# Performance work log

Measured on AMD Instinct MI355X. Metric: run time of the kernel, lower is better.

The kernel has to match this reference:

```python
import jax, jax.numpy as jnp
import numpy as np

N, E, D, H_ATT = 10000, 640000, 128, 64


def setup_inputs() -> dict:
    key = jax.random.key(0)
    ks = jax.random.split(key, 8)
    s = 1.0 / np.sqrt(D)
    return {
        "x": jax.random.normal(ks[0], (N, D), jnp.float32),
        "row": jax.random.randint(ks[1], (E,), 0, N, dtype=jnp.int32),
        "col": jax.random.randint(ks[2], (E,), 0, N, dtype=jnp.int32),
        "W1": jax.random.normal(ks[3], (D, D), jnp.float32) * s,
        "b1": jnp.zeros((D,), jnp.float32),
        "W2": jax.random.normal(ks[4], (D, D), jnp.float32) * s,
        "b2": jnp.zeros((D,), jnp.float32),
        "A1": jax.random.normal(ks[5], (D, H_ATT), jnp.float32) * s,
        "ab1": jnp.zeros((H_ATT,), jnp.float32),
        "A2": jax.random.normal(ks[6], (H_ATT, 1), jnp.float32) * (1.0 / np.sqrt(H_ATT)),
    }


def _cos_sim(a, b):
    # torch.cosine_similarity with eps=1e-8
    num = jnp.sum(a * b, axis=-1)
    den = jnp.maximum(jnp.linalg.norm(a, axis=-1) * jnp.linalg.norm(b, axis=-1), 1e-8)
    return num / den


def _euclid(a, b):
    # nn.PairwiseDistance(p=2)
    return jnp.sqrt(jnp.sum((a - b) ** 2, axis=-1) + 1e-12)


def _gcn(x, ew, row, col, W, b):
    # PyG GCNConv: add self loops (weight 1), symmetric normalization, SpMM.
    n = x.shape[0]
    loop = jnp.arange(n, dtype=row.dtype)
    r = jnp.concatenate([row, loop])  # target
    c = jnp.concatenate([col, loop])  # source
    w = jnp.concatenate([ew, jnp.ones((n,), x.dtype)])
    deg = jax.ops.segment_sum(w, r, num_segments=n)
    dis = jnp.where(deg > 0, jax.lax.rsqrt(jnp.maximum(deg, 1e-12)), 0.0)
    norm = dis[r] * w * dis[c]  # [E+N]
    h = x @ W  # [N, out]
    out = jax.ops.segment_sum(norm[:, None] * h[c], r, num_segments=n)
    return out + b


def reference(x, row, col, W1, b1, W2, b2, A1, ab1, A2):
    # --- cosine branch ---
    w = _cos_sim(x[row], x[col])
    x1 = jax.nn.relu(_gcn(x, w, row, col, W1, b1))
    w = _cos_sim(x1[row], x1[col])
    x1 = _gcn(x1, w, row, col, W2, b2)
    # --- euclidean branch ---
    w = _euclid(x[row], x[col])
    x2 = jax.nn.relu(_gcn(x, w, row, col, W1, b1))
    w = _euclid(x2[row], x2[col])
    x2 = _gcn(x2, w, row, col, W2, b2)
    # --- semantic attention fusion ---
    emb = jnp.stack([x1, x2], axis=1)  # [N, 2, D]
    score = jnp.tanh(emb @ A1 + ab1) @ A2  # [N, 2, 1]
    beta = jax.nn.softmax(score, axis=1)
    return jnp.sum(beta * emb, axis=1)  # [N, D]
```

## Files before the change

kernel.cpp:

```cpp
#include <hip/hip_runtime.h>
#include <cstdint>
#include <cstddef>

#define DF 128
#define HATT 64
#define SL 64
#define RPB 1280

static inline int divup(int a, int b) { return (a + b - 1) / b; }

typedef int vint4 __attribute__((ext_vector_type(4)));

__global__ __launch_bounds__(256) void hist2_kernel(const int* __restrict__ row,
                                                    int* __restrict__ cnt2,
                                                    int E, int n, int ranges, int rpb, int es) {
    int rb = blockIdx.x % ranges;
    int s  = blockIdx.x / ranges;
    int lo = rb * rpb, hi = min(lo + rpb, n);
    int rows = hi - lo;
    __shared__ int lc[RPB];
    for (int j = threadIdx.x; j < rows; j += 256) lc[j] = 0;
    __syncthreads();
    int i0 = s * es, i1 = min(i0 + es, E);
    const vint4* rv = (const vint4*)row;
    for (int j = i0 / 4 + threadIdx.x; j < i1 / 4; j += 256) {
        vint4 r4 = __builtin_nontemporal_load(rv + j);
        if (r4.x >= lo && r4.x < hi) atomicAdd(&lc[r4.x - lo], 1);
        if (r4.y >= lo && r4.y < hi) atomicAdd(&lc[r4.y - lo], 1);
        if (r4.z >= lo && r4.z < hi) atomicAdd(&lc[r4.z - lo], 1);
        if (r4.w >= lo && r4.w < hi) atomicAdd(&lc[r4.w - lo], 1);
    }
    __syncthreads();
    for (int j = threadIdx.x; j < rows; j += 256) cnt2[(size_t)s * n + lo + j] = lc[j];
}

__global__ __launch_bounds__(256) void scanRT_kernel(int* __restrict__ cnt2,
                                                     int* __restrict__ tot, int n) {
    __shared__ int tile[SL][65];
    int r0 = blockIdx.x * 64;
    int w = threadIdx.x >> 6;
    int lane = threadIdx.x & 63;
    int rows = min(64, n - r0);
    for (int s = w; s < SL; s += 4) {
        int v = (lane < rows) ? cnt2[(size_t)s * n + r0 + lane] : 0;
        tile[s][lane] = v;
    }
    __syncthreads();
    int t = threadIdx.x;
    if (t < rows) {
        int run = 0;
#pragma unroll
        for (int s = 0; s < SL; ++s) {
            int v = tile[s][t];
            tile[s][t] = run;
            run += v;
        }
        tot[r0 + t] = run;
    }
    __syncthreads();
    for (int s = w; s < SL; s += 4) {
        if (lane < rows) cnt2[(size_t)s * n + r0 + lane] = tile[s][lane];
    }
}

__global__ __launch_bounds__(1024) void scanT_kernel(const int* __restrict__ tot,
                                                     int* __restrict__ row_ptr, int n) {
    __shared__ int sums[1024];
    int t = threadIdx.x;
    int chunk = (n + 1023) >> 10;
    int start = t * chunk, end = min(start + chunk, n);
    int s = 0;
    for (int r = start; r < end; ++r) s += tot[r];
    sums[t] = s;
    __syncthreads();
    for (int off = 1; off < 1024; off <<= 1) {
        int v = (t >= off) ? sums[t - off] : 0;
        __syncthreads();
        sums[t] += v;
        __syncthreads();
    }
    int run = sums[t] - s;
    for (int r = start; r < end; ++r) {
        row_ptr[r] = run;
        run += tot[r];
    }
    if (t == 1023) row_ptr[n] = sums[1023];
}

__global__ __launch_bounds__(256) void scatter2_kernel(const int* __restrict__ row,
                                                       const int* __restrict__ col,
                                                       const int* __restrict__ cnt2,
                                                       const int* __restrict__ row_ptr,
                                                       unsigned short* __restrict__ col_s,
                                                       int E, int n, int ranges, int rpb, int es) {
    int rb = blockIdx.x % ranges;
    int s  = blockIdx.x / ranges;
    int lo = rb * rpb, hi = min(lo + rpb, n);
    int rows = hi - lo;
    __shared__ int cur[RPB];
    for (int j = threadIdx.x; j < rows; j += 256)
        cur[j] = cnt2[(size_t)s * n + lo + j] + row_ptr[lo + j];
    __syncthreads();
    int i0 = s * es, i1 = min(i0 + es, E);
    const vint4* rv = (const vint4*)row;
    const vint4* cv = (const vint4*)col;
    for (int j = i0 / 4 + threadIdx.x; j < i1 / 4; j += 256) {
        vint4 r4 = __builtin_nontemporal_load(rv + j);
        bool b0 = (r4.x >= lo && r4.x < hi);
        bool b1 = (r4.y >= lo && r4.y < hi);
        bool b2 = (r4.z >= lo && r4.z < hi);
        bool b3 = (r4.w >= lo && r4.w < hi);
        if (b0 | b1 | b2 | b3) {
            vint4 c4 = __builtin_nontemporal_load(cv + j);
            if (b0) { int p = atomicAdd(&cur[r4.x - lo], 1); col_s[p] = (unsigned short)c4.x; }
            if (b1) { int p = atomicAdd(&cur[r4.y - lo], 1); col_s[p] = (unsigned short)c4.y; }
            if (b2) { int p = atomicAdd(&cur[r4.z - lo], 1); col_s[p] = (unsigned short)c4.z; }
            if (b3) { int p = atomicAdd(&cur[r4.w - lo], 1); col_s[p] = (unsigned short)c4.w; }
        }
    }
}

__global__ __launch_bounds__(256) void split_x_kernel(const float* __restrict__ x,
                                                      float* __restrict__ xA,
                                                      float* __restrict__ xB,
                                                      float* __restrict__ sqn, int n) {
    int wid = (blockIdx.x * blockDim.x + threadIdx.x) >> 6;
    int lane = threadIdx.x & 63;
    if (wid >= n) return;
    float v0 = x[(size_t)wid * DF + lane];
    float v1 = x[(size_t)wid * DF + 64 + lane];
    xA[(size_t)wid * 64 + lane] = v0;
    xB[(size_t)wid * 64 + lane] = v1;
    float s = v0 * v0 + v1 * v1;
    for (int off = 32; off; off >>= 1) s += __shfl_xor(s, off);
    if (lane == 0) sqn[wid] = s;
}


__global__ __launch_bounds__(256) void edgewA_kernel(const float* __restrict__ tA,
                                                     const unsigned short* __restrict__ col_s,
                                                     const int* __restrict__ row_ptr,
                                                     float* __restrict__ dpart, int n) {
    int wid = (blockIdx.x * blockDim.x + threadIdx.x) >> 6;
    int lane = threadIdx.x & 63;
    if (wid >= n) return;
    int sub = lane & 15, g = lane >> 4;
    int s = row_ptr[wid], e = row_ptr[wid + 1];
    float4 a = ((const float4*)(tA + (size_t)wid * 64))[sub];
    for (int base = s; base < e; base += 64) {
        int m = e - base; if (m > 64) m = 64;
        int cc = 0;
        if (lane < m) cc = (int)col_s[base + lane];
        float dkeep = 0.f;
#define EWA_BODY(CHK)                                                        \
        _Pragma("unroll")                                                    \
        for (int it = 0; it < 16; ++it) {                                    \
            int idx = g * 16 + it;                                           \
            int c = __shfl(cc, idx);                                         \
            if (CHK) {                                                       \
                float4 b = ((const float4*)(tA + (size_t)c * 64))[sub];      \
                float d = a.x * b.x + a.y * b.y + a.z * b.z + a.w * b.w;     \
                d += __shfl_xor(d, 8); d += __shfl_xor(d, 4);                \
                d += __shfl_xor(d, 2); d += __shfl_xor(d, 1);                \
                dkeep = (sub == it) ? d : dkeep;                             \
            }                                                                \
        }
        if (m == 64) { EWA_BODY(true) } else { EWA_BODY(idx < m) }
#undef EWA_BODY
        if (lane < m) dpart[base + lane] = dkeep;
    }
}

__global__ __launch_bounds__(256) void edgewB1_kernel(const float* __restrict__ tB,
                                                      const float* __restrict__ sqn,
                                                      const unsigned short* __restrict__ col_s,
                                                      const int* __restrict__ row_ptr,
                                                      const float* __restrict__ dpart,
                                                      float* __restrict__ wA,
                                                      float* __restrict__ wB,
                                                      float* __restrict__ disA,
                                                      float* __restrict__ disB, int n) {
    int wid = (blockIdx.x * blockDim.x + threadIdx.x) >> 6;
    int lane = threadIdx.x & 63;
    if (wid >= n) return;
    int sub = lane & 15, g = lane >> 4;
    int s = row_ptr[wid], e = row_ptr[wid + 1];
    float4 a = ((const float4*)(tB + (size_t)wid * 64))[sub];
    float na = sqn[wid];
    float accA = 0.f, accB = 0.f;
    for (int base = s; base < e; base += 64) {
        int m = e - base; if (m > 64) m = 64;
        int cc = 0; float dp = 0.f;
        if (lane < m) {
            cc = (int)col_s[base + lane];
            dp = dpart[base + lane];
        }
        float dkeep = 0.f;
#define EWB1_BODY(CHK)                                                       \
        _Pragma("unroll")                                                    \
        for (int it = 0; it < 16; ++it) {                                    \
            int idx = g * 16 + it;                                           \
            int c = __shfl(cc, idx);                                         \
            if (CHK) {                                                       \
                float4 b = ((const float4*)(tB + (size_t)c * 64))[sub];      \
                float d = a.x * b.x + a.y * b.y + a.z * b.z + a.w * b.w;     \
                d += __shfl_xor(d, 8); d += __shfl_xor(d, 4);                \
                d += __shfl_xor(d, 2); d += __shfl_xor(d, 1);                \
                dkeep = (sub == it) ? d : dkeep;                             \
            }                                                                \
        }
        if (m == 64) { EWB1_BODY(true) } else { EWB1_BODY(idx < m) }
#undef EWB1_BODY
        if (lane < m) {
            float d = dkeep + dp;
            float nb = sqn[cc];
            float cw = d / fmaxf(sqrtf(na * nb), 1e-8f);
            float ew = sqrtf(fmaxf(na + nb - 2.f * d, 0.f) + 1e-12f);
            wA[base + lane] = cw;
            wB[base + lane] = ew;
            accA += cw;
            accB += ew;
        }
    }
#pragma unroll
    for (int off = 32; off; off >>= 1) {
        accA += __shfl_xor(accA, off);
        accB += __shfl_xor(accB, off);
    }
    if (lane == 0) {
        float dA = 1.f + accA;
        disA[wid] = (dA > 0.f) ? rsqrtf(fmaxf(dA, 1e-12f)) : 0.f;
        float dB = 1.f + accB;
        disB[wid] = (dB > 0.f) ? rsqrtf(fmaxf(dB, 1e-12f)) : 0.f;
    }
}

__global__ __launch_bounds__(256) void edgewA2_kernel(const float* __restrict__ t0,
                                                      const float* __restrict__ t1,
                                                      const unsigned short* __restrict__ col_s,
                                                      const int* __restrict__ row_ptr,
                                                      float* __restrict__ dp0,
                                                      float* __restrict__ dp1, int n) {
    int br = blockIdx.x & 1;
    int wid = (blockIdx.x >> 1) * 4 + (threadIdx.x >> 6);
    int lane = threadIdx.x & 63;
    if (wid >= n) return;
    const float* tA = br ? t1 : t0;
    float* dpart = br ? dp1 : dp0;
    int sub = lane & 15, g = lane >> 4;
    int s = row_ptr[wid], e = row_ptr[wid + 1];
    float4 a = ((const float4*)(tA + (size_t)wid * 64))[sub];
    for (int base = s; base < e; base += 64) {
        int m = e - base; if (m > 64) m = 64;
        int cc = 0;
        if (lane < m) cc = (int)col_s[base + lane];
        float dkeep = 0.f;
#define EWA2_BODY(CHK)                                                       \
        _Pragma("unroll")                                                    \
        for (int it = 0; it < 16; ++it) {                                    \
            int idx = g * 16 + it;                                           \
            int c = __shfl(cc, idx);                                         \
            if (CHK) {                                                       \
                float4 b = ((const float4*)(tA + (size_t)c * 64))[sub];      \
                float d = a.x * b.x + a.y * b.y + a.z * b.z + a.w * b.w;     \
                d += __shfl_xor(d, 8); d += __shfl_xor(d, 4);                \
                d += __shfl_xor(d, 2); d += __shfl_xor(d, 1);                \
                dkeep = (sub == it) ? d : dkeep;                             \
            }                                                                \
        }
        if (m == 64) { EWA2_BODY(true) } else { EWA2_BODY(idx < m) }
#undef EWA2_BODY
        if (lane < m) dpart[base + lane] = dkeep;
    }
}

__global__ __launch_bounds__(256) void edgewB2_kernel(const float* __restrict__ t0B,
                                                      const float* __restrict__ t1B,
                                                      const float* __restrict__ sq1pA,
                                                      const float* __restrict__ sq1pB,
                                                      const float* __restrict__ sq2pA,
                                                      const float* __restrict__ sq2pB,
                                                      const unsigned short* __restrict__ col_s,
                                                      const int* __restrict__ row_ptr,
                                                      const float* __restrict__ dp0,
                                                      const float* __restrict__ dp1,
                                                      float* __restrict__ wsA,
                                                      float* __restrict__ wsB,
                                                      float* __restrict__ disA,
                                                      float* __restrict__ disB, int n) {
    int br = blockIdx.x & 1;
    int wid = (blockIdx.x >> 1) * 4 + (threadIdx.x >> 6);
    int lane = threadIdx.x & 63;
    if (wid >= n) return;
    const float* tB = br ? t1B : t0B;
    const float* sqA = br ? sq2pA : sq1pA;
    const float* sqB = br ? sq2pB : sq1pB;
    const float* dpart = br ? dp1 : dp0;
    float* wOut = br ? wsB : wsA;
    float* disOut = br ? disB : disA;
    int sub = lane & 15, g = lane >> 4;
    int s = row_ptr[wid], e = row_ptr[wid + 1];
    float4 a = ((const float4*)(tB + (size_t)wid * 64))[sub];
    float na = sqA[wid] + sqB[wid];
    float acc = 0.f;
    for (int base = s; base < e; base += 64) {
        int m = e - base; if (m > 64) m = 64;
        int cc = 0; float dp = 0.f;
        if (lane < m) {
            cc = (int)col_s[base + lane];
            dp = dpart[base + lane];
        }
        float dkeep = 0.f;
#define EWB2_BODY(CHK)                                                       \
        _Pragma("unroll")                                                    \
        for (int it = 0; it < 16; ++it) {                                    \
            int idx = g * 16 + it;                                           \
            int c = __shfl(cc, idx);                                         \
            if (CHK) {                                                       \
                float4 b = ((const float4*)(tB + (size_t)c * 64))[sub];      \
                float d = a.x * b.x + a.y * b.y + a.z * b.z + a.w * b.w;     \
                d += __shfl_xor(d, 8); d += __shfl_xor(d, 4);                \
                d += __shfl_xor(d, 2); d += __shfl_xor(d, 1);                \
                dkeep = (sub == it) ? d : dkeep;                             \
            }                                                                \
        }
        if (m == 64) { EWB2_BODY(true) } else { EWB2_BODY(idx < m) }
#undef EWB2_BODY
        if (lane < m) {
            float d = dkeep + dp;
            float nb = sqA[cc] + sqB[cc];
            float w;
            if (br == 0) w = d / fmaxf(sqrtf(na * nb), 1e-8f);
            else w = sqrtf(fmaxf(na + nb - 2.f * d, 0.f) + 1e-12f);
            wOut[base + lane] = w;
            acc += w;
        }
    }
#pragma unroll
    for (int off = 32; off; off >>= 1) acc += __shfl_xor(acc, off);
    if (lane == 0) {
        float dg = 1.f + acc;
        disOut[wid] = (dg > 0.f) ? rsqrtf(fmaxf(dg, 1e-12f)) : 0.f;
    }
}

__global__ __launch_bounds__(256) void mm_kernel(const float* __restrict__ inA,
                                                 const float* __restrict__ inB,
                                                 int strideIn,
                                                 const float* __restrict__ W,
                                                 float* __restrict__ hA,
                                                 float* __restrict__ hB, int n) {
    int wid = (blockIdx.x * blockDim.x + threadIdx.x) >> 6;
    int lane = threadIdx.x & 63;
    int i0 = wid * 4;
    if (i0 >= n) return;
    float v0[4], v1[4];
#pragma unroll
    for (int r = 0; r < 4; ++r) {
        int i = i0 + r;
        if (i < n) { v0[r] = inA[(size_t)i * strideIn + lane]; v1[r] = inB[(size_t)i * strideIn + lane]; }
        else { v0[r] = 0.f; v1[r] = 0.f; }
    }
    float acc0[4] = {0.f, 0.f, 0.f, 0.f};
    float acc1[4] = {0.f, 0.f, 0.f, 0.f};
#pragma unroll 4
    for (int k = 0; k < 64; ++k) {
        float w0 = W[k * DF + lane];
        float w1 = W[k * DF + 64 + lane];
#pragma unroll
        for (int r = 0; r < 4; ++r) {
            float a = __shfl(v0[r], k);
            acc0[r] = fmaf(a, w0, acc0[r]);
            acc1[r] = fmaf(a, w1, acc1[r]);
        }
    }
#pragma unroll 4
    for (int k = 0; k < 64; ++k) {
        float w0 = W[(k + 64) * DF + lane];
        float w1 = W[(k + 64) * DF + 64 + lane];
#pragma unroll
        for (int r = 0; r < 4; ++r) {
            float a = __shfl(v1[r], k);
            acc0[r] = fmaf(a, w0, acc0[r]);
            acc1[r] = fmaf(a, w1, acc1[r]);
        }
    }
#pragma unroll
    for (int r = 0; r < 4; ++r) {
        int i = i0 + r;
        if (i < n) { hA[(size_t)i * 64 + lane] = acc0[r]; hB[(size_t)i * 64 + lane] = acc1[r]; }
    }
}

__global__ __launch_bounds__(256) void mm2_kernel(const float* __restrict__ x1A_,
                                                  const float* __restrict__ x1B_,
                                                  const float* __restrict__ x2A_,
                                                  const float* __restrict__ x2B_,
                                                  const float* __restrict__ W,
                                                  float* __restrict__ h1A, float* __restrict__ h1B,
                                                  float* __restrict__ h2A, float* __restrict__ h2B,
                                                  int n) {
    int br = blockIdx.x & 1;
    const float* inA = br ? x2A_ : x1A_;
    const float* inB = br ? x2B_ : x1B_;
    float* hA = br ? h2A : h1A;
    float* hB = br ? h2B : h1B;
    int wid = (blockIdx.x >> 1) * 4 + (threadIdx.x >> 6);
    int lane = threadIdx.x & 63;
    int i0 = wid * 4;
    if (i0 >= n) return;
    float v0[4], v1[4];
#pragma unroll
    for (int r = 0; r < 4; ++r) {
        int i = i0 + r;
        if (i < n) { v0[r] = inA[(size_t)i * 64 + lane]; v1[r] = inB[(size_t)i * 64 + lane]; }
        else { v0[r] = 0.f; v1[r] = 0.f; }
    }
    float acc0[4] = {0.f, 0.f, 0.f, 0.f};
    float acc1[4] = {0.f, 0.f, 0.f, 0.f};
#pragma unroll 4
    for (int k = 0; k < 64; ++k) {
        float w0 = W[k * DF + lane];
        float w1 = W[k * DF + 64 + lane];
#pragma unroll
        for (int r = 0; r < 4; ++r) {
            float a = __shfl(v0[r], k);
            acc0[r] = fmaf(a, w0, acc0[r]);
            acc1[r] = fmaf(a, w1, acc1[r]);
        }
    }
#pragma unroll 4
    for (int k = 0; k < 64; ++k) {
        float w0 = W[(k + 64) * DF + lane];
        float w1 = W[(k + 64) * DF + 64 + lane];
#pragma unroll
        for (int r = 0; r < 4; ++r) {
            float a = __shfl(v1[r], k);
            acc0[r] = fmaf(a, w0, acc0[r]);
            acc1[r] = fmaf(a, w1, acc1[r]);
        }
    }
#pragma unroll
    for (int r = 0; r < 4; ++r) {
        int i = i0 + r;
        if (i < n) { hA[(size_t)i * 64 + lane] = acc0[r]; hB[(size_t)i * 64 + lane] = acc1[r]; }
    }
}

__global__ __launch_bounds__(256) void spmm_l1_kernel(const float* __restrict__ hA,
                                                      const float* __restrict__ hB,
                                                      const float* __restrict__ wsA,
                                                      const float* __restrict__ wsB,
                                                      const unsigned short* __restrict__ col_s,
                                                      const float* __restrict__ disA,
                                                      const float* __restrict__ disB,
                                                      const int* __restrict__ row_ptr,
                                                      const float* __restrict__ bias,
                                                      float* __restrict__ x1A, float* __restrict__ x1B,
                                                      float* __restrict__ x2A, float* __restrict__ x2B,
                                                      float* __restrict__ sq1pA, float* __restrict__ sq1pB,
                                                      float* __restrict__ sq2pA, float* __restrict__ sq2pB,
                                                      int n) {
    int half = blockIdx.x & 1;
    int wid = (blockIdx.x >> 1) * 4 + (threadIdx.x >> 6);
    int lane = threadIdx.x & 63;
    if (wid >= n) return;
    const float* hH = half ? hB : hA;
    float* x1H = half ? x1B : x1A;
    float* x2H = half ? x2B : x2A;
    float* sq1 = half ? sq1pB : sq1pA;
    float* sq2 = half ? sq2pB : sq2pA;
    const float* biasH = bias + half * 64;
    int sub = lane & 15, g = lane >> 4;
    int s = row_ptr[wid], e = row_ptr[wid + 1];
    float diA = disA[wid], diB = disB[wid];
    float4 aA = make_float4(0.f, 0.f, 0.f, 0.f);
    float4 aB = make_float4(0.f, 0.f, 0.f, 0.f);
    for (int base = s; base < e; base += 64) {
        int m = e - base; if (m > 64) m = 64;
        int cc = 0; float wa = 0.f, wb = 0.f;
        if (lane < m) {
            cc = (int)col_s[base + lane];
            wa = wsA[base + lane] * disA[cc];
            wb = wsB[base + lane] * disB[cc];
        }
#define SPL1_BODY(CHK)                                                       \
        _Pragma("unroll")                                                    \
        for (int it = 0; it < 16; ++it) {                                    \
            int idx = it * 4 + g;                                            \
            int c = __shfl(cc, idx);                                         \
            float ceA = __shfl(wa, idx);                                     \
            float ceB = __shfl(wb, idx);                                     \
            if (CHK) {                                                       \
                float4 gv = ((const float4*)(hH + (size_t)c * 64))[sub];     \
                aA.x = fmaf(ceA, gv.x, aA.x); aA.y = fmaf(ceA, gv.y, aA.y);  \
                aA.z = fmaf(ceA, gv.z, aA.z); aA.w = fmaf(ceA, gv.w, aA.w);  \
                aB.x = fmaf(ceB, gv.x, aB.x); aB.y = fmaf(ceB, gv.y, aB.y);  \
                aB.z = fmaf(ceB, gv.z, aB.z); aB.w = fmaf(ceB, gv.w, aB.w);  \
            }                                                                \
        }
        if (m == 64) { SPL1_BODY(true) } else { SPL1_BODY(idx < m) }
#undef SPL1_BODY
    }
#pragma unroll
    for (int off = 16; off <= 32; off <<= 1) {
        aA.x += __shfl_xor(aA.x, off); aA.y += __shfl_xor(aA.y, off);
        aA.z += __shfl_xor(aA.z, off); aA.w += __shfl_xor(aA.w, off);
        aB.x += __shfl_xor(aB.x, off); aB.y += __shfl_xor(aB.y, off);
        aB.z += __shfl_xor(aB.z, off); aB.w += __shfl_xor(aB.w, off);
    }
    float4 hv = ((const float4*)(hH + (size_t)wid * 64))[sub];
    float4 bb = ((const float4*)biasH)[sub];
    float4 oA, oB;
    oA.x = fmaxf(diA * (aA.x + diA * hv.x) + bb.x, 0.f);
    oA.y = fmaxf(diA * (aA.y + diA * hv.y) + bb.y, 0.f);
    oA.z = fmaxf(diA * (aA.z + diA * hv.z) + bb.z, 0.f);
    oA.w = fmaxf(diA * (aA.w + diA * hv.w) + bb.w, 0.f);
    oB.x = fmaxf(diB * (aB.x + diB * hv.x) + bb.x, 0.f);
    oB.y = fmaxf(diB * (aB.y + diB * hv.y) + bb.y, 0.f);
    oB.z = fmaxf(diB * (aB.z + diB * hv.z) + bb.z, 0.f);
    oB.w = fmaxf(diB * (aB.w + diB * hv.w) + bb.w, 0.f);
    if (g == 0) {
        ((float4*)(x1H + (size_t)wid * 64))[sub] = oA;
        ((float4*)(x2H + (size_t)wid * 64))[sub] = oB;
    }
    float sA = oA.x * oA.x + oA.y * oA.y + oA.z * oA.z + oA.w * oA.w;
    float sB = oB.x * oB.x + oB.y * oB.y + oB.z * oB.z + oB.w * oB.w;
#pragma unroll
    for (int off = 8; off; off >>= 1) {
        sA += __shfl_xor(sA, off);
        sB += __shfl_xor(sB, off);
    }
    if (lane == 0) { sq1[wid] = sA; sq2[wid] = sB; }
}

__global__ __launch_bounds__(256) void spmm2q_kernel(const float* __restrict__ h1A,
                                                     const float* __restrict__ h1B,
                                                     const float* __restrict__ h2A,
                                                     const float* __restrict__ h2B,
                                                     const float* __restrict__ wsA,
                                                     const float* __restrict__ wsB,
                                                     const unsigned short* __restrict__ col_s,
                                                     const float* __restrict__ disA,
                                                     const float* __restrict__ disB,
                                                     const int* __restrict__ row_ptr,
                                                     const float* __restrict__ bias,
                                                     float* __restrict__ x1A, float* __restrict__ x1B,
                                                     float* __restrict__ x2A, float* __restrict__ x2B,
                                                     int n) {
    int sel = blockIdx.x & 3;
    int br = sel & 1;
    int half = sel >> 1;
    const float* hH = br ? (half ? h2B : h2A) : (half ? h1B : h1A);
    const float* ws = br ? wsB : wsA;
    const float* dis = br ? disB : disA;
    float* outH = br ? (half ? x2B : x2A) : (half ? x1B : x1A);
    const float* biasH = bias + half * 64;
    int wid = (blockIdx.x >> 2) * 4 + (threadIdx.x >> 6);
    int lane = threadIdx.x & 63;
    if (wid >= n) return;
    int sub = lane & 15, g = lane >> 4;
    int s = row_ptr[wid], e = row_ptr[wid + 1];
    float di = dis[wid];
    float4 a = make_float4(0.f, 0.f, 0.f, 0.f);
    for (int base = s; base < e; base += 64) {
        int m = e - base; if (m > 64) m = 64;
        int cc = 0; float wv = 0.f;
        if (lane < m) {
            cc = (int)col_s[base + lane];
            wv = ws[base + lane] * dis[cc];
        }
#define SP2_BODY(CHK)                                                        \
        _Pragma("unroll")                                                    \
        for (int it = 0; it < 16; ++it) {                                    \
            int idx = it * 4 + g;                                            \
            int c = __shfl(cc, idx);                                         \
            float ce = __shfl(wv, idx);                                      \
            if (CHK) {                                                       \
                float4 gv = ((const float4*)(hH + (size_t)c * 64))[sub];     \
                a.x = fmaf(ce, gv.x, a.x); a.y = fmaf(ce, gv.y, a.y);        \
                a.z = fmaf(ce, gv.z, a.z); a.w = fmaf(ce, gv.w, a.w);        \
            }                                                                \
        }
        if (m == 64) { SP2_BODY(true) } else { SP2_BODY(idx < m) }
#undef SP2_BODY
    }
#pragma unroll
    for (int off = 16; off <= 32; off <<= 1) {
        a.x += __shfl_xor(a.x, off); a.y += __shfl_xor(a.y, off);
        a.z += __shfl_xor(a.z, off); a.w += __shfl_xor(a.w, off);
    }
    if (g == 0) {
        float4 hv = ((const float4*)(hH + (size_t)wid * 64))[sub];
        float4 bb = ((const float4*)biasH)[sub];
        float4 o;
        o.x = di * (a.x + di * hv.x) + bb.x;
        o.y = di * (a.y + di * hv.y) + bb.y;
        o.z = di * (a.z + di * hv.z) + bb.z;
        o.w = di * (a.w + di * hv.w) + bb.w;
        ((float4*)(outH + (size_t)wid * 64))[sub] = o;
    }
}

__global__ __launch_bounds__(256) void attn_kernel(const float* __restrict__ x1A,
                                                   const float* __restrict__ x1B,
                                                   const float* __restrict__ x2A,
                                                   const float* __restrict__ x2B,
                                                   const float* __restrict__ A1,
                                                   const float* __restrict__ ab1,
                                                   const float* __restrict__ A2,
                                                   float* __restrict__ out, int n) {
    __shared__ float sA1[DF * HATT];
    __shared__ float sA2[HATT];
    __shared__ float sab[HATT];
    int tid = threadIdx.x;
    for (int i = tid; i < DF * HATT; i += 256) sA1[i] = A1[i];
    if (tid < HATT) { sA2[tid] = A2[tid]; sab[tid] = ab1[tid]; }
    __syncthreads();
    int lane = tid & 63;
    int wib = tid >> 6;
    int wid = blockIdx.x * 4 + wib;
    int nw = gridDim.x * 4;
    for (int i = wid; i < n; i += nw) {
        float u0 = x1A[(size_t)i * 64 + lane], u1 = x1B[(size_t)i * 64 + lane];
        float v0 = x2A[(size_t)i * 64 + lane], v1 = x2B[(size_t)i * 64 + lane];
        float acc1 = 0.f, acc2 = 0.f;
#pragma unroll 4
        for (int d = 0; d < 64; ++d) {
            float w = sA1[d * HATT + lane];
            acc1 = fmaf(__shfl(u0, d), w, acc1);
            acc2 = fmaf(__shfl(v0, d), w, acc2);
        }
#pragma unroll 4
        for (int d = 0; d < 64; ++d) {
            float w = sA1[(d + 64) * HATT + lane];
            acc1 = fmaf(__shfl(u1, d), w, acc1);
            acc2 = fmaf(__shfl(v1, d), w, acc2);
        }
        float t1 = tanhf(acc1 + sab[lane]) * sA2[lane];
        float t2 = tanhf(acc2 + sab[lane]) * sA2[lane];
        for (int off = 32; off; off >>= 1) {
            t1 += __shfl_xor(t1, off);
            t2 += __shfl_xor(t2, off);
        }
        float mx = fmaxf(t1, t2);
        float e1 = expf(t1 - mx), e2 = expf(t2 - mx);
        float inv = 1.f / (e1 + e2);
        float be1 = e1 * inv, be2 = e2 * inv;
        out[(size_t)i * DF + lane] = be1 * u0 + be2 * v0;
        out[(size_t)i * DF + 64 + lane] = be1 * u1 + be2 * v1;
    }
}


extern "C" void kernel_launch(void* const* d_in, const int* in_sizes, int n_in,
                              void* d_out, int out_size, void* d_ws, size_t ws_size,
                              hipStream_t stream) {
    const float* x  = (const float*)d_in[0];
    const int* row  = (const int*)d_in[1];
    const int* col  = (const int*)d_in[2];
    const float* W1 = (const float*)d_in[3];
    const float* b1 = (const float*)d_in[4];
    const float* W2 = (const float*)d_in[5];
    const float* b2 = (const float*)d_in[6];
    const float* A1 = (const float*)d_in[7];
    const float* ab1= (const float*)d_in[8];
    const float* A2 = (const float*)d_in[9];
    const int N = in_sizes[0] / DF;
    const int E = in_sizes[1];
    float* out = (float*)d_out;

    char* p = (char*)d_ws;
    auto alloc_b = [&](size_t bytes) -> char* {
        char* r = p;
        p += (bytes + 255) & ~(size_t)255;
        return r;
    };
    float* xA    = (float*)alloc_b((size_t)N * 64 * 4);
    float* xB    = (float*)alloc_b((size_t)N * 64 * 4);
    float* hA    = (float*)alloc_b((size_t)N * 64 * 4);
    float* hB    = (float*)alloc_b((size_t)N * 64 * 4);
    float* h2A   = (float*)alloc_b((size_t)N * 64 * 4);
    float* h2B   = (float*)alloc_b((size_t)N * 64 * 4);
    float* x1A   = (float*)alloc_b((size_t)N * 64 * 4);
    float* x1B   = (float*)alloc_b((size_t)N * 64 * 4);
    float* x2A   = (float*)alloc_b((size_t)N * 64 * 4);
    float* x2B   = (float*)alloc_b((size_t)N * 64 * 4);
    float* wsA   = (float*)alloc_b((size_t)E * 4);
    float* wsB   = (float*)alloc_b((size_t)E * 4);
    float* dp0   = (float*)alloc_b((size_t)E * 4);
    float* dp1   = (float*)alloc_b((size_t)E * 4);
    float* disA  = (float*)alloc_b((size_t)N * 4);
    float* disB  = (float*)alloc_b((size_t)N * 4);
    float* sqnx  = (float*)alloc_b((size_t)N * 4);
    float* sq1pA = (float*)alloc_b((size_t)N * 4);
    float* sq1pB = (float*)alloc_b((size_t)N * 4);
    float* sq2pA = (float*)alloc_b((size_t)N * 4);
    float* sq2pB = (float*)alloc_b((size_t)N * 4);
    int* cnt2    = (int*)alloc_b((size_t)SL * N * 4);
    int* tot     = (int*)alloc_b((size_t)N * 4);
    int* rowptr  = (int*)alloc_b((size_t)(N + 1) * 4);
    unsigned short* col_s = (unsigned short*)alloc_b((size_t)E * 2);
    (void)ws_size; (void)n_in; (void)out_size;

    const int nodeBlocks  = divup(N * 64, 256);
    const int pairBlocks  = 2 * nodeBlocks;
    const int quadBlocks  = 4 * nodeBlocks;
    const int mmBlocks    = divup(divup(N, 4), 4);
    const int mm2Blocks   = 2 * mmBlocks;
    const int ranges = divup(N, RPB);
    const int rpb    = divup(N, ranges);
    int es = divup(E, SL); es = (es + 3) & ~3;
    const int prepBlocks = ranges * SL;

    hist2_kernel<<<prepBlocks, 256, 0, stream>>>(row, cnt2, E, N, ranges, rpb, es);
    split_x_kernel<<<nodeBlocks, 256, 0, stream>>>(x, xA, xB, sqnx, N);
    scanRT_kernel<<<divup(N, 64), 256, 0, stream>>>(cnt2, tot, N);
    scanT_kernel<<<1, 1024, 0, stream>>>(tot, rowptr, N);
    scatter2_kernel<<<prepBlocks, 256, 0, stream>>>(row, col, cnt2, rowptr, col_s, E, N, ranges, rpb, es);

    mm_kernel<<<mmBlocks, 256, 0, stream>>>(x, x + 64, DF, W1, hA, hB, N);

    edgewA_kernel<<<nodeBlocks, 256, 0, stream>>>(xA, col_s, rowptr, dp0, N);
    edgewB1_kernel<<<nodeBlocks, 256, 0, stream>>>(xB, sqnx, col_s, rowptr, dp0,
                                                   wsA, wsB, disA, disB, N);

    spmm_l1_kernel<<<pairBlocks, 256, 0, stream>>>(hA, hB, wsA, wsB, col_s, disA, disB,
                                                   rowptr, b1, x1A, x1B, x2A, x2B,
                                                   sq1pA, sq1pB, sq2pA, sq2pB, N);

    edgewA2_kernel<<<pairBlocks, 256, 0, stream>>>(x1A, x2A, col_s, rowptr, dp0, dp1, N);
    edgewB2_kernel<<<pairBlocks, 256, 0, stream>>>(x1B, x2B, sq1pA, sq1pB, sq2pA, sq2pB,
                                                   col_s, rowptr, dp0, dp1,
                                                   wsA, wsB, disA, disB, N);

    mm2_kernel<<<mm2Blocks, 256, 0, stream>>>(x1A, x1B, x2A, x2B, W2, hA, hB, h2A, h2B, N);

    spmm2q_kernel<<<quadBlocks, 256, 0, stream>>>(hA, hB, h2A, h2B, wsA, wsB, col_s,
                                                  disA, disB, rowptr, b2,
                                                  x1A, x1B, x2A, x2B, N);

    attn_kernel<<<divup(N, 4), 256, 0, stream>>>(x1A, x1B, x2A, x2B, A1, ab1, A2, out, N);
}
```

Measured before the change: 358.1 us.

## Co-launch independent kernels in merged grids and prewarm gather tables in cache

Independent kernel pairs share one launch through block-index dispatch: histogram with x split, first edge-weight pass with the layer-1 matmul, and second edge-weight pass with the layer-2 matmul. This removes launch gaps and lets the work overlap. Each gather kernel also starts by streaming a slice of its feature table with coalesced float4 loads into a discarded sum, so the later random row gathers hit L2. The warming adds extra reads per block, and the merged grids mix block types that need different resources, which can hurt occupancy.

```diff
diff --git a/kernel.cpp b/kernel.cpp
--- a/kernel.cpp
+++ b/kernel.cpp
@@ -11,11 +11,23 @@
 
 typedef int vint4 __attribute__((ext_vector_type(4)));
 
-__global__ __launch_bounds__(256) void hist2_kernel(const int* __restrict__ row,
-                                                    int* __restrict__ cnt2,
-                                                    int E, int n, int ranges, int rpb, int es) {
-    int rb = blockIdx.x % ranges;
-    int s  = blockIdx.x / ranges;
+__device__ __forceinline__ void warm_table(const float* t, int nf4, int b, int nb) {
+    int slice = (nf4 + nb - 1) / nb;
+    int start = b * slice;
+    int end = min(start + slice, nf4);
+    float acc = 0.f;
+    for (int i = start + (int)threadIdx.x; i < end; i += 256) {
+        float4 v = ((const float4*)t)[i];
+        acc += v.x + v.y + v.z + v.w;
+    }
+    asm volatile("" :: "v"(acc));
+}
+
+__device__ __forceinline__ void hist2_body(int bid, const int* __restrict__ row,
+                                           int* __restrict__ cnt2,
+                                           int E, int n, int ranges, int rpb, int es) {
+    int rb = bid % ranges;
+    int s  = bid / ranges;
     int lo = rb * rpb, hi = min(lo + rpb, n);
     int rows = hi - lo;
     __shared__ int lc[RPB];
@@ -32,6 +44,36 @@
     }
     __syncthreads();
     for (int j = threadIdx.x; j < rows; j += 256) cnt2[(size_t)s * n + lo + j] = lc[j];
+}
+
+__device__ __forceinline__ void split_x_body(int bid, const float* __restrict__ x,
+                                             float* __restrict__ xA,
+                                             float* __restrict__ xB,
+                                             float* __restrict__ sqn, int n) {
+    int wid = bid * 4 + (threadIdx.x >> 6);
+    int lane = threadIdx.x & 63;
+    if (wid >= n) return;
+    float v0 = x[(size_t)wid * DF + lane];
+    float v1 = x[(size_t)wid * DF + 64 + lane];
+    xA[(size_t)wid * 64 + lane] = v0;
+    xB[(size_t)wid * 64 + lane] = v1;
+    float s = v0 * v0 + v1 * v1;
+    for (int off = 32; off; off >>= 1) s += __shfl_xor(s, off);
+    if (lane == 0) sqn[wid] = s;
+}
+
+__global__ __launch_bounds__(256) void prep_split_kernel(const int* __restrict__ row,
+                                                         int* __restrict__ cnt2,
+                                                         const float* __restrict__ x,
+                                                         float* __restrict__ xA,
+                                                         float* __restrict__ xB,
+                                                         float* __restrict__ sqn,
+                                                         int E, int n, int ranges, int rpb,
+                                                         int es, int prepBlocks) {
+    if ((int)blockIdx.x < prepBlocks)
+        hist2_body(blockIdx.x, row, cnt2, E, n, ranges, rpb, es);
+    else
+        split_x_body(blockIdx.x - prepBlocks, x, xA, xB, sqn, n);
 }
 
 __global__ __launch_bounds__(256) void scanRT_kernel(int* __restrict__ cnt2,
@@ -120,28 +162,12 @@
     }
 }
 
-__global__ __launch_bounds__(256) void split_x_kernel(const float* __restrict__ x,
-                                                      float* __restrict__ xA,
-                                                      float* __restrict__ xB,
-                                                      float* __restrict__ sqn, int n) {
-    int wid = (blockIdx.x * blockDim.x + threadIdx.x) >> 6;
-    int lane = threadIdx.x & 63;
-    if (wid >= n) return;
-    float v0 = x[(size_t)wid * DF + lane];
-    float v1 = x[(size_t)wid * DF + 64 + lane];
-    xA[(size_t)wid * 64 + lane] = v0;
-    xB[(size_t)wid * 64 + lane] = v1;
-    float s = v0 * v0 + v1 * v1;
-    for (int off = 32; off; off >>= 1) s += __shfl_xor(s, off);
-    if (lane == 0) sqn[wid] = s;
-}
-
-
-__global__ __launch_bounds__(256) void edgewA_kernel(const float* __restrict__ tA,
-                                                     const unsigned short* __restrict__ col_s,
-                                                     const int* __restrict__ row_ptr,
-                                                     float* __restrict__ dpart, int n) {
-    int wid = (blockIdx.x * blockDim.x + threadIdx.x) >> 6;
+__device__ __forceinline__ void edgewA_body(int bid, const float* __restrict__ tA,
+                                            const unsigned short* __restrict__ col_s,
+                                            const int* __restrict__ row_ptr,
+                                            float* __restrict__ dpart, int n, int nbTable) {
+    warm_table(tA, n * 16, bid, nbTable);
+    int wid = bid * 4 + (threadIdx.x >> 6);
     int lane = threadIdx.x & 63;
     if (wid >= n) return;
     int sub = lane & 15, g = lane >> 4;
@@ -171,6 +197,67 @@
     }
 }
 
+__device__ __forceinline__ void mm_body(int bid, const float* __restrict__ inA,
+                                        const float* __restrict__ inB, int strideIn,
+                                        const float* __restrict__ W,
+                                        float* __restrict__ hA, float* __restrict__ hB, int n) {
+    int wid = bid * 4 + (threadIdx.x >> 6);
+    int lane = threadIdx.x & 63;
+    int i0 = wid * 4;
+    if (i0 >= n) return;
+    float v0[4], v1[4];
+#pragma unroll
+    for (int r = 0; r < 4; ++r) {
+        int i = i0 + r;
+        if (i < n) { v0[r] = inA[(size_t)i * strideIn + lane]; v1[r] = inB[(size_t)i * strideIn + lane]; }
+        else { v0[r] = 0.f; v1[r] = 0.f; }
+    }
+    float acc0[4] = {0.f, 0.f, 0.f, 0.f};
+    float acc1[4] = {0.f, 0.f, 0.f, 0.f};
+#pragma unroll 4
+    for (int k = 0; k < 64; ++k) {
+        float w0 = W[k * DF + lane];
+        float w1 = W[k * DF + 64 + lane];
+#pragma unroll
+        for (int r = 0; r < 4; ++r) {
+            float a = __shfl(v0[r], k);
+            acc0[r] = fmaf(a, w0, acc0[r]);
+            acc1[r] = fmaf(a, w1, acc1[r]);
+        }
+    }
+#pragma unroll 4
+    for (int k = 0; k < 64; ++k) {
+        float w0 = W[(k + 64) * DF + lane];
+        float w1 = W[(k + 64) * DF + 64 + lane];
+#pragma unroll
+        for (int r = 0; r < 4; ++r) {
+            float a = __shfl(v1[r], k);
+            acc0[r] = fmaf(a, w0, acc0[r]);
+            acc1[r] = fmaf(a, w1, acc1[r]);
+        }
+    }
+#pragma unroll
+    for (int r = 0; r < 4; ++r) {
+        int i = i0 + r;
+        if (i < n) { hA[(size_t)i * 64 + lane] = acc0[r]; hB[(size_t)i * 64 + lane] = acc1[r]; }
+    }
+}
+
+__global__ __launch_bounds__(256) void ew1mm_kernel(const float* __restrict__ xA,
+                                                    const unsigned short* __restrict__ col_s,
+                                                    const int* __restrict__ row_ptr,
+                                                    float* __restrict__ dp0,
+                                                    const float* __restrict__ x,
+                                                    const float* __restrict__ W1,
+                                                    float* __restrict__ hA,
+                                                    float* __restrict__ hB,
+                                                    int n, int nodeBlocks) {
+    if ((int)blockIdx.x < nodeBlocks)
+        edgewA_body(blockIdx.x, xA, col_s, row_ptr, dp0, n, nodeBlocks);
+    else
+        mm_body(blockIdx.x - nodeBlocks, x, x + 64, DF, W1, hA, hB, n);
+}
+
 __global__ __launch_bounds__(256) void edgewB1_kernel(const float* __restrict__ tB,
                                                       const float* __restrict__ sqn,
                                                       const unsigned short* __restrict__ col_s,
@@ -179,8 +266,9 @@
                                                       float* __restrict__ wA,
                                                       float* __restrict__ wB,
                                                       float* __restrict__ disA,
-                                                      float* __restrict__ disB, int n) {
-    int wid = (blockIdx.x * blockDim.x + threadIdx.x) >> 6;
+                                                      float* __restrict__ disB, int n, int nbTable) {
+    warm_table(tB, n * 16, blockIdx.x, nbTable);
+    int wid = blockIdx.x * 4 + (threadIdx.x >> 6);
     int lane = threadIdx.x & 63;
     if (wid >= n) return;
     int sub = lane & 15, g = lane >> 4;
@@ -235,218 +323,6 @@
     }
 }
 
-__global__ __launch_bounds__(256) void edgewA2_kernel(const float* __restrict__ t0,
-                                                      const float* __restrict__ t1,
-                                                      const unsigned short* __restrict__ col_s,
-                                                      const int* __restrict__ row_ptr,
-                                                      float* __restrict__ dp0,
-                                                      float* __restrict__ dp1, int n) {
-    int br = blockIdx.x & 1;
-    int wid = (blockIdx.x >> 1) * 4 + (threadIdx.x >> 6);
-    int lane = threadIdx.x & 63;
-    if (wid >= n) return;
-    const float* tA = br ? t1 : t0;
-    float* dpart = br ? dp1 : dp0;
-    int sub = lane & 15, g = lane >> 4;
-    int s = row_ptr[wid], e = row_ptr[wid + 1];
-    float4 a = ((const float4*)(tA + (size_t)wid * 64))[sub];
-    for (int base = s; base < e; base += 64) {
-        int m = e - base; if (m > 64) m = 64;
-        int cc = 0;
-        if (lane < m) cc = (int)col_s[base + lane];
-        float dkeep = 0.f;
-#define EWA2_BODY(CHK)                                                       \
-        _Pragma("unroll")                                                    \
-        for (int it = 0; it < 16; ++it) {                                    \
-            int idx = g * 16 + it;                                           \
-            int c = __shfl(cc, idx);                                         \
-            if (CHK) {                                                       \
-                float4 b = ((const float4*)(tA + (size_t)c * 64))[sub];      \
-                float d = a.x * b.x + a.y * b.y + a.z * b.z + a.w * b.w;     \
-                d += __shfl_xor(d, 8); d += __shfl_xor(d, 4);                \
-                d += __shfl_xor(d, 2); d += __shfl_xor(d, 1);                \
-                dkeep = (sub == it) ? d : dkeep;                             \
-            }                                                                \
-        }
-        if (m == 64) { EWA2_BODY(true) } else { EWA2_BODY(idx < m) }
-#undef EWA2_BODY
-        if (lane < m) dpart[base + lane] = dkeep;
-    }
-}
-
-__global__ __launch_bounds__(256) void edgewB2_kernel(const float* __restrict__ t0B,
-                                                      const float* __restrict__ t1B,
-                                                      const float* __restrict__ sq1pA,
-                                                      const float* __restrict__ sq1pB,
-                                                      const float* __restrict__ sq2pA,
-                                                      const float* __restrict__ sq2pB,
-                                                      const unsigned short* __restrict__ col_s,
-                                                      const int* __restrict__ row_ptr,
-                                                      const float* __restrict__ dp0,
-                                                      const float* __restrict__ dp1,
-                                                      float* __restrict__ wsA,
-                                                      float* __restrict__ wsB,
-                                                      float* __restrict__ disA,
-                                                      float* __restrict__ disB, int n) {
-    int br = blockIdx.x & 1;
-    int wid = (blockIdx.x >> 1) * 4 + (threadIdx.x >> 6);
-    int lane = threadIdx.x & 63;
-    if (wid >= n) return;
-    const float* tB = br ? t1B : t0B;
-    const float* sqA = br ? sq2pA : sq1pA;
-    const float* sqB = br ? sq2pB : sq1pB;
-    const float* dpart = br ? dp1 : dp0;
-    float* wOut = br ? wsB : wsA;
-    float* disOut = br ? disB : disA;
-    int sub = lane & 15, g = lane >> 4;
-    int s = row_ptr[wid], e = row_ptr[wid + 1];
-    float4 a = ((const float4*)(tB + (size_t)wid * 64))[sub];
-    float na = sqA[wid] + sqB[wid];
-    float acc = 0.f;
-    for (int base = s; base < e; base += 64) {
-        int m = e - base; if (m > 64) m = 64;
-        int cc = 0; float dp = 0.f;
-        if (lane < m) {
-            cc = (int)col_s[base + lane];
-            dp = dpart[base + lane];
-        }
-        float dkeep = 0.f;
-#define EWB2_BODY(CHK)                                                       \
-        _Pragma("unroll")                                                    \
-        for (int it = 0; it < 16; ++it) {                                    \
-            int idx = g * 16 + it;                                           \
-            int c = __shfl(cc, idx);                                         \
-            if (CHK) {                                                       \
-                float4 b = ((const float4*)(tB + (size_t)c * 64))[sub];      \
-                float d = a.x * b.x + a.y * b.y + a.z * b.z + a.w * b.w;     \
-                d += __shfl_xor(d, 8); d += __shfl_xor(d, 4);                \
-                d += __shfl_xor(d, 2); d += __shfl_xor(d, 1);                \
-                dkeep = (sub == it) ? d : dkeep;                             \
-            }                                                                \
-        }
-        if (m == 64) { EWB2_BODY(true) } else { EWB2_BODY(idx < m) }
-#undef EWB2_BODY
-        if (lane < m) {
-            float d = dkeep + dp;
-            float nb = sqA[cc] + sqB[cc];
-            float w;
-            if (br == 0) w = d / fmaxf(sqrtf(na * nb), 1e-8f);
-            else w = sqrtf(fmaxf(na + nb - 2.f * d, 0.f) + 1e-12f);
-            wOut[base + lane] = w;
-            acc += w;
-        }
-    }
-#pragma unroll
-    for (int off = 32; off; off >>= 1) acc += __shfl_xor(acc, off);
-    if (lane == 0) {
-        float dg = 1.f + acc;
-        disOut[wid] = (dg > 0.f) ? rsqrtf(fmaxf(dg, 1e-12f)) : 0.f;
-    }
-}
-
-__global__ __launch_bounds__(256) void mm_kernel(const float* __restrict__ inA,
-                                                 const float* __restrict__ inB,
-                                                 int strideIn,
-                                                 const float* __restrict__ W,
-                                                 float* __restrict__ hA,
-                                                 float* __restrict__ hB, int n) {
-    int wid = (blockIdx.x * blockDim.x + threadIdx.x) >> 6;
-    int lane = threadIdx.x & 63;
-    int i0 = wid * 4;
-    if (i0 >= n) return;
-    float v0[4], v1[4];
-#pragma unroll
-    for (int r = 0; r < 4; ++r) {
-        int i = i0 + r;
-        if (i < n) { v0[r] = inA[(size_t)i * strideIn + lane]; v1[r] = inB[(size_t)i * strideIn + lane]; }
-        else { v0[r] = 0.f; v1[r] = 0.f; }
-    }
-    float acc0[4] = {0.f, 0.f, 0.f, 0.f};
-    float acc1[4] = {0.f, 0.f, 0.f, 0.f};
-#pragma unroll 4
-    for (int k = 0; k < 64; ++k) {
-        float w0 = W[k * DF + lane];
-        float w1 = W[k * DF + 64 + lane];
-#pragma unroll
-        for (int r = 0; r < 4; ++r) {
-            float a = __shfl(v0[r], k);
-            acc0[r] = fmaf(a, w0, acc0[r]);
-            acc1[r] = fmaf(a, w1, acc1[r]);
-        }
-    }
-#pragma unroll 4
-    for (int k = 0; k < 64; ++k) {
-        float w0 = W[(k + 64) * DF + lane];
-        float w1 = W[(k + 64) * DF + 64 + lane];
-#pragma unroll
-        for (int r = 0; r < 4; ++r) {
-            float a = __shfl(v1[r], k);
-            acc0[r] = fmaf(a, w0, acc0[r]);
-            acc1[r] = fmaf(a, w1, acc1[r]);
-        }
-    }
-#pragma unroll
-    for (int r = 0; r < 4; ++r) {
-        int i = i0 + r;
-        if (i < n) { hA[(size_t)i * 64 + lane] = acc0[r]; hB[(size_t)i * 64 + lane] = acc1[r]; }
-    }
-}
-
-__global__ __launch_bounds__(256) void mm2_kernel(const float* __restrict__ x1A_,
-                                                  const float* __restrict__ x1B_,
-                                                  const float* __restrict__ x2A_,
-                                                  const float* __restrict__ x2B_,
-                                                  const float* __restrict__ W,
-                                                  float* __restrict__ h1A, float* __restrict__ h1B,
-                                                  float* __restrict__ h2A, float* __restrict__ h2B,
-                                                  int n) {
-    int br = blockIdx.x & 1;
-    const float* inA = br ? x2A_ : x1A_;
-    const float* inB = br ? x2B_ : x1B_;
-    float* hA = br ? h2A : h1A;
-    float* hB = br ? h2B : h1B;
-    int wid = (blockIdx.x >> 1) * 4 + (threadIdx.x >> 6);
-    int lane = threadIdx.x & 63;
-    int i0 = wid * 4;
-    if (i0 >= n) return;
-    float v0[4], v1[4];
-#pragma unroll
-    for (int r = 0; r < 4; ++r) {
-        int i = i0 + r;
-        if (i < n) { v0[r] = inA[(size_t)i * 64 + lane]; v1[r] = inB[(size_t)i * 64 + lane]; }
-        else { v0[r] = 0.f; v1[r] = 0.f; }
-    }
-    float acc0[4] = {0.f, 0.f, 0.f, 0.f};
-    float acc1[4] = {0.f, 0.f, 0.f, 0.f};
-#pragma unroll 4
-    for (int k = 0; k < 64; ++k) {
-        float w0 = W[k * DF + lane];
-        float w1 = W[k * DF + 64 + lane];
-#pragma unroll
-        for (int r = 0; r < 4; ++r) {
-            float a = __shfl(v0[r], k);
-            acc0[r] = fmaf(a, w0, acc0[r]);
-            acc1[r] = fmaf(a, w1, acc1[r]);
-        }
-    }
-#pragma unroll 4
-    for (int k = 0; k < 64; ++k) {
-        float w0 = W[(k + 64) * DF + lane];
-        float w1 = W[(k + 64) * DF + 64 + lane];
-#pragma unroll
-        for (int r = 0; r < 4; ++r) {
-            float a = __shfl(v1[r], k);
-            acc0[r] = fmaf(a, w0, acc0[r]);
-            acc1[r] = fmaf(a, w1, acc1[r]);
-        }
-    }
-#pragma unroll
-    for (int r = 0; r < 4; ++r) {
-        int i = i0 + r;
-        if (i < n) { hA[(size_t)i * 64 + lane] = acc0[r]; hB[(size_t)i * 64 + lane] = acc1[r]; }
-    }
-}
-
 __global__ __launch_bounds__(256) void spmm_l1_kernel(const float* __restrict__ hA,
                                                       const float* __restrict__ hB,
                                                       const float* __restrict__ wsA,
@@ -460,12 +336,13 @@
                                                       float* __restrict__ x2A, float* __restrict__ x2B,
                                                       float* __restrict__ sq1pA, float* __restrict__ sq1pB,
                                                       float* __restrict__ sq2pA, float* __restrict__ sq2pB,
-                                                      int n) {
+                                                      int n, int nbTable) {
     int half = blockIdx.x & 1;
+    const float* hH = half ? hB : hA;
+    warm_table(hH, n * 16, blockIdx.x >> 1, nbTable);
     int wid = (blockIdx.x >> 1) * 4 + (threadIdx.x >> 6);
     int lane = threadIdx.x & 63;
     if (wid >= n) return;
-    const float* hH = half ? hB : hA;
     float* x1H = half ? x1B : x1A;
     float* x2H = half ? x2B : x2A;
     float* sq1 = half ? sq1pB : sq1pA;
@@ -534,6 +411,114 @@
     if (lane == 0) { sq1[wid] = sA; sq2[wid] = sB; }
 }
 
+__device__ __forceinline__ void mm2_body(int bid, const float* __restrict__ x1A_,
+                                         const float* __restrict__ x1B_,
+                                         const float* __restrict__ x2A_,
+                                         const float* __restrict__ x2B_,
+                                         const float* __restrict__ W,
+                                         float* __restrict__ h1A, float* __restrict__ h1B,
+                                         float* __restrict__ h2A, float* __restrict__ h2B, int n) {
+    int br = bid & 1;
+    const float* inA = br ? x2A_ : x1A_;
+    const float* inB = br ? x2B_ : x1B_;
+    float* hA = br ? h2A : h1A;
+    float* hB = br ? h2B : h1B;
+    mm_body(bid >> 1, inA, inB, 64, W, hA, hB, n);
+}
+
+__global__ __launch_bounds__(256) void ew2mm_kernel(const float* __restrict__ x1A,
+                                                    const float* __restrict__ x1B,
+                                                    const float* __restrict__ x2A,
+                                                    const float* __restrict__ x2B,
+                                                    const unsigned short* __restrict__ col_s,
+                                                    const int* __restrict__ row_ptr,
+                                                    float* __restrict__ dp0,
+                                                    float* __restrict__ dp1,
+                                                    const float* __restrict__ W2,
+                                                    float* __restrict__ h1A, float* __restrict__ h1B,
+                                                    float* __restrict__ h2A, float* __restrict__ h2B,
+                                                    int n, int pairBlocks, int nodeBlocks) {
+    if ((int)blockIdx.x < pairBlocks) {
+        int br = blockIdx.x & 1;
+        const float* tA = br ? x2A : x1A;
+        float* dpart = br ? dp1 : dp0;
+        edgewA_body(blockIdx.x >> 1, tA, col_s, row_ptr, dpart, n, nodeBlocks);
+    } else {
+        mm2_body(blockIdx.x - pairBlocks, x1A, x1B, x2A, x2B, W2, h1A, h1B, h2A, h2B, n);
+    }
+}
+
+__global__ __launch_bounds__(256) void edgewB2_kernel(const float* __restrict__ t0B,
+                                                      const float* __restrict__ t1B,
+                                                      const float* __restrict__ sq1pA,
+                                                      const float* __restrict__ sq1pB,
+                                                      const float* __restrict__ sq2pA,
+                                                      const float* __restrict__ sq2pB,
+                                                      const unsigned short* __restrict__ col_s,
+                                                      const int* __restrict__ row_ptr,
+                                                      const float* __restrict__ dp0,
+                                                      const float* __restrict__ dp1,
+                                                      float* __restrict__ wsA,
+                                                      float* __restrict__ wsB,
+                                                      float* __restrict__ disA,
+                                                      float* __restrict__ disB, int n, int nbTable) {
+    int br = blockIdx.x & 1;
+    const float* tB = br ? t1B : t0B;
+    warm_table(tB, n * 16, blockIdx.x >> 1, nbTable);
+    int wid = (blockIdx.x >> 1) * 4 + (threadIdx.x >> 6);
+    int lane = threadIdx.x & 63;
+    if (wid >= n) return;
+    const float* sqA = br ? sq2pA : sq1pA;
+    const float* sqB = br ? sq2pB : sq1pB;
+    const float* dpart = br ? dp1 : dp0;
+    float* wOut = br ? wsB : wsA;
+    float* disOut = br ? disB : disA;
+    int sub = lane & 15, g = lane >> 4;
+    int s = row_ptr[wid], e = row_ptr[wid + 1];
+    float4 a = ((const float4*)(tB + (size_t)wid * 64))[sub];
+    float na = sqA[wid] + sqB[wid];
+    float acc = 0.f;
+    for (int base = s; base < e; base += 64) {
+        int m = e - base; if (m > 64) m = 64;
+        int cc = 0; float dp = 0.f;
+        if (lane < m) {
+            cc = (int)col_s[base + lane];
+            dp = dpart[base + lane];
+        }
+        float dkeep = 0.f;
+#define EWB2_BODY(CHK)                                                       \
+        _Pragma("unroll")                                                    \
+        for (int it = 0; it < 16; ++it) {                                    \
+            int idx = g * 16 + it;                                           \
+            int c = __shfl(cc, idx);                                         \
+            if (CHK) {                                                       \
+                float4 b = ((const float4*)(tB + (size_t)c * 64))[sub];      \
+                float d = a.x * b.x + a.y * b.y + a.z * b.z + a.w * b.w;     \
+                d += __shfl_xor(d, 8); d += __shfl_xor(d, 4);                \
+                d += __shfl_xor(d, 2); d += __shfl_xor(d, 1);                \
+                dkeep = (sub == it) ? d : dkeep;                             \
+            }                                                                \
+        }
+        if (m == 64) { EWB2_BODY(true) } else { EWB2_BODY(idx < m) }
+#undef EWB2_BODY
+        if (lane < m) {
+            float d = dkeep + dp;
+            float nb = sqA[cc] + sqB[cc];
+            float w;
+            if (br == 0) w = d / fmaxf(sqrtf(na * nb), 1e-8f);
+            else w = sqrtf(fmaxf(na + nb - 2.f * d, 0.f) + 1e-12f);
+            wOut[base + lane] = w;
+            acc += w;
+        }
+    }
+#pragma unroll
+    for (int off = 32; off; off >>= 1) acc += __shfl_xor(acc, off);
+    if (lane == 0) {
+        float dg = 1.f + acc;
+        disOut[wid] = (dg > 0.f) ? rsqrtf(fmaxf(dg, 1e-12f)) : 0.f;
+    }
+}
+
 __global__ __launch_bounds__(256) void spmm2q_kernel(const float* __restrict__ h1A,
                                                      const float* __restrict__ h1B,
                                                      const float* __restrict__ h2A,
@@ -547,11 +532,12 @@
                                                      const float* __restrict__ bias,
                                                      float* __restrict__ x1A, float* __restrict__ x1B,
                                                      float* __restrict__ x2A, float* __restrict__ x2B,
-                                                     int n) {
+                                                     int n, int nbTable) {
     int sel = blockIdx.x & 3;
     int br = sel & 1;
     int half = sel >> 1;
     const float* hH = br ? (half ? h2B : h2A) : (half ? h1B : h1A);
+    warm_table(hH, n * 16, blockIdx.x >> 2, nbTable);
     const float* ws = br ? wsB : wsA;
     const float* dis = br ? disB : disA;
     float* outH = br ? (half ? x2B : x2A) : (half ? x1B : x1A);
@@ -713,32 +699,33 @@
     int es = divup(E, SL); es = (es + 3) & ~3;
     const int prepBlocks = ranges * SL;
 
-    hist2_kernel<<<prepBlocks, 256, 0, stream>>>(row, cnt2, E, N, ranges, rpb, es);
-    split_x_kernel<<<nodeBlocks, 256, 0, stream>>>(x, xA, xB, sqnx, N);
+    prep_split_kernel<<<prepBlocks + nodeBlocks, 256, 0, stream>>>(row, cnt2, x, xA, xB, sqnx,
+                                                                   E, N, ranges, rpb, es, prepBlocks);
     scanRT_kernel<<<divup(N, 64), 256, 0, stream>>>(cnt2, tot, N);
     scanT_kernel<<<1, 1024, 0, stream>>>(tot, rowptr, N);
     scatter2_kernel<<<prepBlocks, 256, 0, stream>>>(row, col, cnt2, rowptr, col_s, E, N, ranges, rpb, es);
 
-    mm_kernel<<<mmBlocks, 256, 0, stream>>>(x, x + 64, DF, W1, hA, hB, N);
-
-    edgewA_kernel<<<nodeBlocks, 256, 0, stream>>>(xA, col_s, rowptr, dp0, N);
+    ew1mm_kernel<<<nodeBlocks + mmBlocks, 256, 0, stream>>>(xA, col_s, rowptr, dp0,
+                                                            x, W1, hA, hB, N, nodeBlocks);
+
     edgewB1_kernel<<<nodeBlocks, 256, 0, stream>>>(xB, sqnx, col_s, rowptr, dp0,
-                                                   wsA, wsB, disA, disB, N);
+                                                   wsA, wsB, disA, disB, N, nodeBlocks);
 
     spmm_l1_kernel<<<pairBlocks, 256, 0, stream>>>(hA, hB, wsA, wsB, col_s, disA, disB,
                                                    rowptr, b1, x1A, x1B, x2A, x2B,
-                                                   sq1pA, sq1pB, sq2pA, sq2pB, N);
-
-    edgewA2_kernel<<<pairBlocks, 256, 0, stream>>>(x1A, x2A, col_s, rowptr, dp0, dp1, N);
+                                                   sq1pA, sq1pB, sq2pA, sq2pB, N, nodeBlocks);
+
+    ew2mm_kernel<<<pairBlocks + mm2Blocks, 256, 0, stream>>>(x1A, x1B, x2A, x2B, col_s, rowptr,
+                                                             dp0, dp1, W2, hA, hB, h2A, h2B,
+                                                             N, pairBlocks, nodeBlocks);
+
     edgewB2_kernel<<<pairBlocks, 256, 0, stream>>>(x1B, x2B, sq1pA, sq1pB, sq2pA, sq2pB,
                                                    col_s, rowptr, dp0, dp1,
-                                                   wsA, wsB, disA, disB, N);
-
-    mm2_kernel<<<mm2Blocks, 256, 0, stream>>>(x1A, x1B, x2A, x2B, W2, hA, hB, h2A, h2B, N);
+                                                   wsA, wsB, disA, disB, N, nodeBlocks);
 
     spmm2q_kernel<<<quadBlocks, 256, 0, stream>>>(hA, hB, h2A, h2B, wsA, wsB, col_s,
                                                   disA, disB, rowptr, b2,
-                                                  x1A, x1B, x2A, x2B, N);
+                                                  x1A, x1B, x2A, x2B, N, nodeBlocks);
 
     attn_kernel<<<divup(N, 4), 256, 0, stream>>>(x1A, x1B, x2A, x2B, A1, ab1, A2, out, N);
 }
```

Result: no change. 358.7 us (+0.2%).
